# Optimization experiments

Measured on AMD Instinct MI355X. Metric: run time of the kernel, lower is better.

Reference implementation:

```python
import jax, jax.numpy as jnp
import numpy as np
import math

B, S, D, H = 2, 2048, 1024, 16
DK = D // H


def setup_inputs() -> dict:
    key = jax.random.key(0)
    ks = jax.random.split(key, 12)
    std = 1.0 / math.sqrt(D)
    inp = {
        "query": jax.random.normal(ks[0], (B, S, D), jnp.float32),
        "key_": jax.random.normal(ks[1], (B, S, D), jnp.float32),
        "value": jax.random.normal(ks[2], (B, S, D), jnp.float32),
        # causal mask: True = masked out
        "attn_mask": jnp.triu(jnp.ones((S, S), jnp.bool_), k=1),
        "w_q": jax.random.uniform(ks[3], (D, D), jnp.float32, -std, std),
        "b_q": jax.random.uniform(ks[4], (D,), jnp.float32, -std, std),
        "w_k": jax.random.uniform(ks[5], (D, D), jnp.float32, -std, std),
        "b_k": jax.random.uniform(ks[6], (D,), jnp.float32, -std, std),
        "w_v": jax.random.uniform(ks[7], (D, D), jnp.float32, -std, std),
        "b_v": jax.random.uniform(ks[8], (D,), jnp.float32, -std, std),
        "w_o": jax.random.uniform(ks[9], (D, D), jnp.float32, -std, std),
        "b_o": jax.random.uniform(ks[10], (D,), jnp.float32, -std, std),
    }
    return inp


def reference(query, key_, value, attn_mask, w_q, b_q, w_k, b_k, w_v, b_v, w_o, b_o):
    # linear projections (torch Linear: x @ W.T + b)
    q = query @ w_q.T + b_q
    k = key_ @ w_k.T + b_k
    v = value @ w_v.T + b_v
    # [B, H, S, DK]
    q = q.reshape(B, S, H, DK).transpose(0, 2, 1, 3)
    k = k.reshape(B, S, H, DK).transpose(0, 2, 1, 3)
    v = v.reshape(B, S, H, DK).transpose(0, 2, 1, 3)
    scores = jnp.einsum("bhqd,bhkd->bhqk", q, k) / jnp.sqrt(jnp.float32(DK))
    scores = jnp.where(attn_mask[None, None, :, :], -jnp.inf, scores)
    attn = jax.nn.softmax(scores, axis=-1)
    context = jnp.einsum("bhqk,bhkd->bhqd", attn, v)
    context = context.transpose(0, 2, 1, 3).reshape(B, S, D)
    return context @ w_o.T + b_o
```

## Files before the change

### kernel.cpp

```cpp
#include <hip/hip_runtime.h>

#define B_ 2
#define S_ 2048
#define D_ 1024
#define H_ 16
#define DK_ 64
#define K_ 1024

typedef __bf16 bf16x8 __attribute__((ext_vector_type(8)));
typedef __bf16 bf16x4 __attribute__((ext_vector_type(4)));
typedef float f32x4 __attribute__((ext_vector_type(4)));

#define QSCALE 0.18033688011112042f

__device__ __forceinline__ void gload16(const void* g, void* l) {
    __builtin_amdgcn_global_load_lds(
        (const __attribute__((address_space(1))) unsigned int*)g,
        (__attribute__((address_space(3))) unsigned int*)l, 16, 0, 0);
}

__device__ __forceinline__ bf16x8 cvt8f(const float* __restrict__ p) {
    f32x4 a = *reinterpret_cast<const f32x4*>(p);
    f32x4 b = *reinterpret_cast<const f32x4*>(p + 4);
    bf16x8 r;
#pragma unroll
    for (int j = 0; j < 4; ++j) { r[j] = (__bf16)a[j]; r[j + 4] = (__bf16)b[j]; }
    return r;
}

__global__ __launch_bounds__(256) void cvt_all(
    const float* __restrict__ s0, const float* __restrict__ s1, const float* __restrict__ s2,
    const float* __restrict__ s3, const float* __restrict__ s4, const float* __restrict__ s5,
    const float* __restrict__ s6,
    __bf16* __restrict__ d0, __bf16* __restrict__ d1, __bf16* __restrict__ d2,
    __bf16* __restrict__ d3, __bf16* __restrict__ d4, __bf16* __restrict__ d5,
    __bf16* __restrict__ d6)
{
    const int y = blockIdx.y;
    const float* s; __bf16* d; int n8;
    const int n8_big = (B_ * S_ * D_) / 8, n8_w = (D_ * D_) / 8;
    switch (y) {
        case 0: s = s0; d = d0; n8 = n8_big; break;
        case 1: s = s1; d = d1; n8 = n8_big; break;
        case 2: s = s2; d = d2; n8 = n8_big; break;
        case 3: s = s3; d = d3; n8 = n8_w; break;
        case 4: s = s4; d = d4; n8 = n8_w; break;
        case 5: s = s5; d = d5; n8 = n8_w; break;
        default: s = s6; d = d6; n8 = n8_w; break;
    }
    int i = blockIdx.x * 256 + threadIdx.x;
    if (i >= n8) return;
    *reinterpret_cast<bf16x8*>(d + (size_t)i * 8) = cvt8f(s + (size_t)i * 8);
}

__global__ __launch_bounds__(256) void gemm_qkv(
    const __bf16* __restrict__ qin, const __bf16* __restrict__ kin, const __bf16* __restrict__ vin,
    const __bf16* __restrict__ wq,  const __bf16* __restrict__ wk,  const __bf16* __restrict__ wv,
    const float* __restrict__ bq,   const float* __restrict__ bk,   const float* __restrict__ bv,
    __bf16* __restrict__ qo, __bf16* __restrict__ ko, __bf16* __restrict__ vto)
{
    __shared__ __attribute__((aligned(16))) __bf16 ldsA[2 * 128 * 32];
    __shared__ __attribute__((aligned(16))) __bf16 ldsB[2 * 128 * 32];

    const int z = blockIdx.z;
    const __bf16* A; const __bf16* Bm;
    int brow, bcol;
    if (z == 0)      { A = qin; Bm = wq;  brow = blockIdx.x * 128; bcol = blockIdx.y * 128; }
    else if (z == 1) { A = kin; Bm = wk;  brow = blockIdx.x * 128; bcol = blockIdx.y * 128; }
    else             { A = wv;  Bm = vin;
                       brow = (blockIdx.x & 7) * 128;
                       bcol = (blockIdx.y * 4 + (blockIdx.x >> 3)) * 128; }

    const int tid = threadIdx.x;
    const int w = tid >> 6, lane = tid & 63;
    const int l15 = lane & 15, lh = lane >> 4;
    const int wr = w >> 1, wc = w & 1;
    const int srow  = lane >> 2;
    const int scolb = (((lane & 3) ^ ((lane >> 3) & 3))) * 16;
    const char* Ab = (const char*)A;
    const char* Bb = (const char*)Bm;

    auto stage = [&](int buf, int k0) {
#pragma unroll
        for (int c = 0; c < 2; ++c) {
            const int chunk = w * 2 + c;
            const int row   = chunk * 16 + srow;
            const int loff  = __builtin_amdgcn_readfirstlane(buf * 8192 + chunk * 1024);
            gload16(Ab + (size_t)(brow + row) * 2048 + k0 * 2 + scolb, (char*)ldsA + loff);
            gload16(Bb + (size_t)(bcol + row) * 2048 + k0 * 2 + scolb, (char*)ldsB + loff);
        }
    };

    const int rsw = ((l15 >> 1) & 3);

    f32x4 acc[4][4] = {};
    stage(0, 0);
    int buf = 0;
    for (int k0 = 0; k0 < K_; k0 += 32) {
        if (k0 + 32 < K_) {
            stage(buf ^ 1, k0 + 32);
            asm volatile("s_waitcnt vmcnt(4)" ::: "memory");
        } else {
            asm volatile("s_waitcnt vmcnt(0)" ::: "memory");
        }
        __builtin_amdgcn_s_barrier();
        __builtin_amdgcn_sched_barrier(0);

        const int bo = buf * 8192;
        bf16x8 af[4], bfr[4];
#pragma unroll
        for (int m = 0; m < 4; ++m) {
            const int row = wr * 64 + m * 16 + l15;
            af[m] = *reinterpret_cast<const bf16x8*>(
                (const char*)ldsA + bo + row * 64 + ((lh ^ rsw) * 16));
        }
#pragma unroll
        for (int n = 0; n < 4; ++n) {
            const int row = wc * 64 + n * 16 + l15;
            bfr[n] = *reinterpret_cast<const bf16x8*>(
                (const char*)ldsB + bo + row * 64 + ((lh ^ rsw) * 16));
        }

        __builtin_amdgcn_s_setprio(1);
#pragma unroll
        for (int m = 0; m < 4; ++m)
#pragma unroll
            for (int n = 0; n < 4; ++n)
                acc[m][n] = __builtin_amdgcn_mfma_f32_16x16x32_bf16(bfr[n], af[m], acc[m][n], 0, 0, 0);
        __builtin_amdgcn_s_setprio(0);

        __builtin_amdgcn_s_barrier();
        buf ^= 1;
    }

    if (z < 2) {
        const float* bias = (z == 0) ? bq : bk;
        __bf16* o = (z == 0) ? qo : ko;
        const int hh  = (bcol >> 6) + wc;
#pragma unroll
        for (int ni = 0; ni < 4; ++ni) {
            const int n4  = bcol + wc * 64 + ni * 16 + lh * 4;
            const f32x4 b4 = *reinterpret_cast<const f32x4*>(bias + n4);
            const int dk4 = ni * 16 + lh * 4;
#pragma unroll
            for (int mi = 0; mi < 4; ++mi) {
                const int m  = brow + wr * 64 + mi * 16 + l15;
                const int bb = m >> 11, ss = m & (S_ - 1);
                bf16x4 pk;
#pragma unroll
                for (int r = 0; r < 4; ++r) {
                    float v = acc[mi][ni][r] + b4[r];
                    if (z == 0) v *= QSCALE;
                    pk[r] = (__bf16)v;
                }
                *reinterpret_cast<bf16x4*>(
                    o + (((size_t)(bb * H_ + hh)) * S_ + ss) * DK_ + dk4) = pk;
            }
        }
    } else {
#pragma unroll
        for (int mi = 0; mi < 4; ++mi) {
            const int m  = brow + wr * 64 + mi * 16 + l15;
            const int hh = m >> 6, dk = m & 63;
            const float bias = bv[m];
#pragma unroll
            for (int ni = 0; ni < 4; ++ni) {
                const int n4 = bcol + wc * 64 + ni * 16 + lh * 4;
                const int bb = n4 >> 11, ss = n4 & (S_ - 1);
                bf16x4 pk;
#pragma unroll
                for (int r = 0; r < 4; ++r)
                    pk[r] = (__bf16)(acc[mi][ni][r] + bias);
                *reinterpret_cast<bf16x4*>(
                    vto + (((size_t)(bb * H_ + hh)) * DK_ + dk) * S_ + ss) = pk;
            }
        }
    }
}

__global__ __launch_bounds__(256) void gemm_out(
    const __bf16* __restrict__ A, const __bf16* __restrict__ Bm,
    const float* __restrict__ bias, float* __restrict__ out)
{
    __shared__ __attribute__((aligned(16))) __bf16 ldsA[2 * 128 * 32];
    __shared__ __attribute__((aligned(16))) __bf16 ldsB[2 * 128 * 32];

    const int tid = threadIdx.x;
    const int w = tid >> 6, lane = tid & 63;
    const int l15 = lane & 15, lh = lane >> 4;
    const int wr = w >> 1, wc = w & 1;
    const int brow = blockIdx.x * 128;
    const int bcol = blockIdx.y * 128;
    const int srow  = lane >> 2;
    const int scolb = (((lane & 3) ^ ((lane >> 3) & 3))) * 16;
    const char* Ab = (const char*)A;
    const char* Bb = (const char*)Bm;

    auto stage = [&](int buf, int k0) {
#pragma unroll
        for (int c = 0; c < 2; ++c) {
            const int chunk = w * 2 + c;
            const int row   = chunk * 16 + srow;
            const int loff  = __builtin_amdgcn_readfirstlane(buf * 8192 + chunk * 1024);
            gload16(Ab + (size_t)(brow + row) * 2048 + k0 * 2 + scolb, (char*)ldsA + loff);
            gload16(Bb + (size_t)(bcol + row) * 2048 + k0 * 2 + scolb, (char*)ldsB + loff);
        }
    };

    const int rsw = ((l15 >> 1) & 3);

    f32x4 acc[4][4] = {};
    stage(0, 0);
    int buf = 0;
    for (int k0 = 0; k0 < K_; k0 += 32) {
        if (k0 + 32 < K_) {
            stage(buf ^ 1, k0 + 32);
            asm volatile("s_waitcnt vmcnt(4)" ::: "memory");
        } else {
            asm volatile("s_waitcnt vmcnt(0)" ::: "memory");
        }
        __builtin_amdgcn_s_barrier();
        __builtin_amdgcn_sched_barrier(0);

        const int bo = buf * 8192;
        bf16x8 af[4], bfr[4];
#pragma unroll
        for (int m = 0; m < 4; ++m) {
            const int row = wr * 64 + m * 16 + l15;
            af[m] = *reinterpret_cast<const bf16x8*>(
                (const char*)ldsA + bo + row * 64 + ((lh ^ rsw) * 16));
        }
#pragma unroll
        for (int n = 0; n < 4; ++n) {
            const int row = wc * 64 + n * 16 + l15;
            bfr[n] = *reinterpret_cast<const bf16x8*>(
                (const char*)ldsB + bo + row * 64 + ((lh ^ rsw) * 16));
        }

        __builtin_amdgcn_s_setprio(1);
#pragma unroll
        for (int m = 0; m < 4; ++m)
#pragma unroll
            for (int n = 0; n < 4; ++n)
                acc[m][n] = __builtin_amdgcn_mfma_f32_16x16x32_bf16(bfr[n], af[m], acc[m][n], 0, 0, 0);
        __builtin_amdgcn_s_setprio(0);

        __builtin_amdgcn_s_barrier();
        buf ^= 1;
    }

#pragma unroll
    for (int ni = 0; ni < 4; ++ni) {
        const int n4 = bcol + wc * 64 + ni * 16 + lh * 4;
        const f32x4 b4 = *reinterpret_cast<const f32x4*>(bias + n4);
#pragma unroll
        for (int mi = 0; mi < 4; ++mi) {
            const int m = brow + wr * 64 + mi * 16 + l15;
            f32x4 v;
#pragma unroll
            for (int r = 0; r < 4; ++r) v[r] = acc[mi][ni][r] + b4[r];
            *reinterpret_cast<f32x4*>(out + (size_t)m * D_ + n4) = v;
        }
    }
}

__global__ __launch_bounds__(256, 4) void attn_kernel(
    const __bf16* __restrict__ Q, const __bf16* __restrict__ K,
    const __bf16* __restrict__ VT, __bf16* __restrict__ CTX)
{
    __shared__ __attribute__((aligned(16))) char ldsK[2][8192];
    __shared__ __attribute__((aligned(16))) char ldsV[2][8192];
    __shared__ __attribute__((aligned(16))) __bf16 p_lds[4][16][64];

    const int tid = threadIdx.x;
    const int w = tid >> 6, l = tid & 63;
    const int l15 = l & 15, lh = l >> 4;

    const int c  = blockIdx.x & 255;
    const int rr = blockIdx.x >> 8;
    const int qq = c >> 5;
    const int bhidx = c & 31;
    int panel;
    if (rr == 0)      panel = 31 - qq;
    else if (rr == 1) panel = qq;
    else if (rr == 2) panel = 23 - qq;
    else              panel = 8 + qq;
    const int h = bhidx & 15;
    const int b = bhidx >> 4;

    const size_t bh = (size_t)(b * H_ + h);
    const __bf16* qp   = Q + bh * S_ * DK_;
    const char*  kbase = (const char*)(K  + bh * S_ * DK_);
    const char*  vbase = (const char*)(VT + bh * DK_ * S_);

    const int np = panel + 1;
    const int wave_base = panel * 64 + w * 16;

    const int srow = l >> 3;
    const int ssw  = ((l & 7) * 16) ^ (srow * 16);

    auto stage = [&](int pos) {
        const int k0 = pos * 64;
        char* lk = ldsK[pos & 1];
        char* lv = ldsV[pos & 1];
#pragma unroll
        for (int i = 0; i < 2; ++i) {
            const int r0   = w * 16 + i * 8;
            const int loff = __builtin_amdgcn_readfirstlane(r0 * 128);
            gload16(kbase + (size_t)(k0 + r0 + srow) * 128 + ssw, lk + loff);
            gload16(vbase + (size_t)(r0 + srow) * 4096 + (size_t)k0 * 2 + ssw, lv + loff);
        }
    };

    bf16x8 aq[2];
#pragma unroll
    for (int cc = 0; cc < 2; ++cc)
        aq[cc] = *reinterpret_cast<const bf16x8*>(
            qp + (size_t)(wave_base + l15) * DK_ + cc * 32 + lh * 8);

    bf16x8 vones;
#pragma unroll
    for (int j = 0; j < 8; ++j) vones[j] = (__bf16)1.0f;
    const f32x4 fzero = {0.f, 0.f, 0.f, 0.f};

    f32x4 acc[4] = {};
    f32x4 acc_l = {};
    float mrun = -INFINITY;

    stage(0);

    for (int it = 0; it < np; ++it) {
        if (it + 1 < np) {
            stage(it + 1);
            asm volatile("s_waitcnt vmcnt(4)" ::: "memory");
        } else {
            asm volatile("s_waitcnt vmcnt(0)" ::: "memory");
        }
        __builtin_amdgcn_s_barrier();
        __builtin_amdgcn_sched_barrier(0);

        const int k0 = it * 64;
        const char* lk = ldsK[it & 1];
        const char* lv = ldsV[it & 1];

        bf16x8 ak[4][2];
#pragma unroll
        for (int t = 0; t < 4; ++t)
#pragma unroll
            for (int cc = 0; cc < 2; ++cc) {
                const int col = (cc * 64 + lh * 16) ^ ((l15 & 7) << 4);
                ak[t][cc] = *reinterpret_cast<const bf16x8*>(lk + (t * 16 + l15) * 128 + col);
            }

        f32x4 sacc[4];
        __builtin_amdgcn_s_setprio(1);
#pragma unroll
        for (int t = 0; t < 4; ++t) {
            sacc[t] = __builtin_amdgcn_mfma_f32_16x16x32_bf16(ak[t][0], aq[0], fzero, 0, 0, 0);
            sacc[t] = __builtin_amdgcn_mfma_f32_16x16x32_bf16(ak[t][1], aq[1], sacc[t], 0, 0, 0);
        }
        __builtin_amdgcn_s_setprio(0);

        bf16x8 bv[4][2];
#pragma unroll
        for (int nt = 0; nt < 4; ++nt)
#pragma unroll
            for (int c2 = 0; c2 < 2; ++c2) {
                const int col = (c2 * 64 + lh * 16) ^ ((l15 & 7) << 4);
                bv[nt][c2] = *reinterpret_cast<const bf16x8*>(lv + (nt * 16 + l15) * 128 + col);
            }

        if (k0 + 63 > wave_base) {
            const int qa = wave_base + l15;
#pragma unroll
            for (int t = 0; t < 4; ++t)
#pragma unroll
                for (int r = 0; r < 4; ++r) {
                    const int ka = k0 + t * 16 + lh * 4 + r;
                    if (ka > qa) sacc[t][r] = -INFINITY;
                }
        }

        f32x4 m4 = sacc[0];
#pragma unroll
        for (int t = 1; t < 4; ++t)
#pragma unroll
            for (int r = 0; r < 4; ++r) m4[r] = fmaxf(m4[r], sacc[t][r]);
        float rm = fmaxf(fmaxf(m4[0], m4[1]), fmaxf(m4[2], m4[3]));
        rm = fmaxf(rm, __shfl_xor(rm, 16, 64));
        rm = fmaxf(rm, __shfl_xor(rm, 32, 64));

        if (!__all(rm <= mrun + 8.f)) {
            const float mnew = fmaxf(mrun, rm);
            const float scl  = exp2f(mrun - mnew);
            mrun = mnew;
#pragma unroll
            for (int r = 0; r < 4; ++r) {
                const float sr = __shfl(scl, lh * 4 + r, 64);
#pragma unroll
                for (int nt = 0; nt < 4; ++nt) acc[nt][r] *= sr;
                acc_l[r] *= sr;
            }
        }

#pragma unroll
        for (int t = 0; t < 4; ++t) {
            bf16x4 pk;
#pragma unroll
            for (int r = 0; r < 4; ++r)
                pk[r] = (__bf16)exp2f(sacc[t][r] - mrun);
            const int wcol = (t * 16 + lh * 4) ^ ((l15 & 7) << 3);
            *reinterpret_cast<bf16x4*>(&p_lds[w][l15][wcol]) = pk;
        }

        bf16x8 pa[2];
#pragma unroll
        for (int c2 = 0; c2 < 2; ++c2) {
            const int rcol = (c2 * 32 + lh * 8) ^ ((l15 & 7) << 3);
            pa[c2] = *reinterpret_cast<const bf16x8*>(&p_lds[w][l15][rcol]);
        }

        __builtin_amdgcn_s_setprio(1);
#pragma unroll
        for (int nt = 0; nt < 4; ++nt)
#pragma unroll
            for (int c2 = 0; c2 < 2; ++c2)
                acc[nt] = __builtin_amdgcn_mfma_f32_16x16x32_bf16(
                    pa[c2], bv[nt][c2], acc[nt], 0, 0, 0);
        acc_l = __builtin_amdgcn_mfma_f32_16x16x32_bf16(pa[0], vones, acc_l, 0, 0, 0);
        acc_l = __builtin_amdgcn_mfma_f32_16x16x32_bf16(pa[1], vones, acc_l, 0, 0, 0);
        __builtin_amdgcn_s_setprio(0);

        __builtin_amdgcn_s_barrier();
    }

#pragma unroll
    for (int r = 0; r < 4; ++r) {
        const float linv = 1.f / acc_l[r];
        const int srow2 = wave_base + lh * 4 + r;
#pragma unroll
        for (int nt = 0; nt < 4; ++nt)
            CTX[((size_t)b * S_ + srow2) * D_ + h * DK_ + nt * 16 + l15] =
                (__bf16)(acc[nt][r] * linv);
    }
}

extern "C" void kernel_launch(void* const* d_in, const int* in_sizes, int n_in,
                              void* d_out, int out_size, void* d_ws, size_t ws_size,
                              hipStream_t stream) {
    (void)in_sizes; (void)n_in; (void)out_size; (void)ws_size;

    const float* query = (const float*)d_in[0];
    const float* key_  = (const float*)d_in[1];
    const float* value = (const float*)d_in[2];
    const float* w_q = (const float*)d_in[4];
    const float* b_q = (const float*)d_in[5];
    const float* w_k = (const float*)d_in[6];
    const float* b_k = (const float*)d_in[7];
    const float* w_v = (const float*)d_in[8];
    const float* b_v = (const float*)d_in[9];
    const float* w_o = (const float*)d_in[10];
    const float* b_o = (const float*)d_in[11];
    float* out = (float*)d_out;

    char* Wp = (char*)d_ws;
    const size_t MB = 1024 * 1024;
    __bf16* qin = (__bf16*)(Wp + 0 * MB);
    __bf16* kin = (__bf16*)(Wp + 8 * MB);
    __bf16* vin = (__bf16*)(Wp + 16 * MB);
    __bf16* wq  = (__bf16*)(Wp + 24 * MB);
    __bf16* wk  = (__bf16*)(Wp + 26 * MB);
    __bf16* wv  = (__bf16*)(Wp + 28 * MB);
    __bf16* wo  = (__bf16*)(Wp + 30 * MB);
    __bf16* q   = (__bf16*)(Wp + 32 * MB);
    __bf16* k   = (__bf16*)(Wp + 40 * MB);
    __bf16* vt  = (__bf16*)(Wp + 48 * MB);
    __bf16* ctx = qin;

    const int n8_big = (B_ * S_ * D_) / 8;

    hipLaunchKernelGGL(cvt_all, dim3(n8_big / (256 * 8) * 8, 7), dim3(256), 0, stream,
                       query, key_, value, w_q, w_k, w_v, w_o,
                       qin, kin, vin, wq, wk, wv, wo);
    hipLaunchKernelGGL(gemm_qkv, dim3(32, 8, 3), dim3(256), 0, stream,
                       qin, kin, vin, wq, wk, wv, b_q, b_k, b_v, q, k, vt);
    hipLaunchKernelGGL(attn_kernel, dim3(1024), dim3(256), 0, stream,
                       q, k, vt, ctx);
    hipLaunchKernelGGL(gemm_out, dim3(32, 8), dim3(256), 0, stream,
                       ctx, wo, b_o, out);
}
```

Baseline: 131.0 us.

## Triple-buffer GEMM LDS pipeline and remap workgroups across XCDs

Both projection GEMMs now use three LDS buffers with a prefetch distance of two K-tiles. This drops the trailing barrier in each iteration, so only one barrier per K-step remains. The grids are flattened to 1D, and block IDs are remapped so that consecutive tiles land on the same XCD (wg&7 chiplet interleave), which is meant to improve L2 reuse of shared A/B panels. The cost is 48KB of LDS per block instead of 32KB, which may reduce occupancy.

Measured after the change: 133.5 us. No clear change (+1.9%).

```diff
diff --git a/kernel.cpp b/kernel.cpp
--- a/kernel.cpp
+++ b/kernel.cpp
@@ -59,17 +59,23 @@
     const float* __restrict__ bq,   const float* __restrict__ bk,   const float* __restrict__ bv,
     __bf16* __restrict__ qo, __bf16* __restrict__ ko, __bf16* __restrict__ vto)
 {
-    __shared__ __attribute__((aligned(16))) __bf16 ldsA[2 * 128 * 32];
-    __shared__ __attribute__((aligned(16))) __bf16 ldsB[2 * 128 * 32];
-
-    const int z = blockIdx.z;
+    __shared__ __attribute__((aligned(16))) char ldsA[3 * 8192];
+    __shared__ __attribute__((aligned(16))) char ldsB[3 * 8192];
+
+    const int wg   = blockIdx.x;
+    const int wgid = (wg & 7) * 96 + (wg >> 3);
+    const int z    = wgid >> 8;
+    const int rem  = wgid & 255;
+    const int by   = rem >> 5;
+    const int bx   = rem & 31;
+
     const __bf16* A; const __bf16* Bm;
     int brow, bcol;
-    if (z == 0)      { A = qin; Bm = wq;  brow = blockIdx.x * 128; bcol = blockIdx.y * 128; }
-    else if (z == 1) { A = kin; Bm = wk;  brow = blockIdx.x * 128; bcol = blockIdx.y * 128; }
+    if (z == 0)      { A = qin; Bm = wq;  brow = bx * 128; bcol = by * 128; }
+    else if (z == 1) { A = kin; Bm = wk;  brow = bx * 128; bcol = by * 128; }
     else             { A = wv;  Bm = vin;
-                       brow = (blockIdx.x & 7) * 128;
-                       bcol = (blockIdx.y * 4 + (blockIdx.x >> 3)) * 128; }
+                       brow = (bx & 7) * 128;
+                       bcol = (by * 4 + (bx >> 3)) * 128; }
 
     const int tid = threadIdx.x;
     const int w = tid >> 6, lane = tid & 63;
@@ -80,45 +86,46 @@
     const char* Ab = (const char*)A;
     const char* Bb = (const char*)Bm;
 
-    auto stage = [&](int buf, int k0) {
+    auto stage = [&](int tt, int buf) {
+        const int k0 = tt * 32;
 #pragma unroll
         for (int c = 0; c < 2; ++c) {
             const int chunk = w * 2 + c;
             const int row   = chunk * 16 + srow;
             const int loff  = __builtin_amdgcn_readfirstlane(buf * 8192 + chunk * 1024);
-            gload16(Ab + (size_t)(brow + row) * 2048 + k0 * 2 + scolb, (char*)ldsA + loff);
-            gload16(Bb + (size_t)(bcol + row) * 2048 + k0 * 2 + scolb, (char*)ldsB + loff);
+            gload16(Ab + (size_t)(brow + row) * 2048 + k0 * 2 + scolb, ldsA + loff);
+            gload16(Bb + (size_t)(bcol + row) * 2048 + k0 * 2 + scolb, ldsB + loff);
         }
     };
 
     const int rsw = ((l15 >> 1) & 3);
-
     f32x4 acc[4][4] = {};
-    stage(0, 0);
-    int buf = 0;
-    for (int k0 = 0; k0 < K_; k0 += 32) {
-        if (k0 + 32 < K_) {
-            stage(buf ^ 1, k0 + 32);
-            asm volatile("s_waitcnt vmcnt(4)" ::: "memory");
-        } else {
-            asm volatile("s_waitcnt vmcnt(0)" ::: "memory");
-        }
+    const int NT = K_ / 32;
+
+    stage(0, 0); stage(1, 1);
+    int cur = 0;
+    for (int t = 0; t < NT; ++t) {
+        if (t + 1 < NT) { asm volatile("s_waitcnt vmcnt(4)" ::: "memory"); }
+        else            { asm volatile("s_waitcnt vmcnt(0)" ::: "memory"); }
         __builtin_amdgcn_s_barrier();
         __builtin_amdgcn_sched_barrier(0);
 
-        const int bo = buf * 8192;
+        if (t + 2 < NT) {
+            const int sbuf = (cur == 0) ? 2 : cur - 1;
+            stage(t + 2, sbuf);
+        }
+
+        const int bo = cur * 8192;
         bf16x8 af[4], bfr[4];
 #pragma unroll
         for (int m = 0; m < 4; ++m) {
             const int row = wr * 64 + m * 16 + l15;
-            af[m] = *reinterpret_cast<const bf16x8*>(
-                (const char*)ldsA + bo + row * 64 + ((lh ^ rsw) * 16));
+            af[m] = *reinterpret_cast<const bf16x8*>(ldsA + bo + row * 64 + ((lh ^ rsw) * 16));
         }
 #pragma unroll
         for (int n = 0; n < 4; ++n) {
             const int row = wc * 64 + n * 16 + l15;
-            bfr[n] = *reinterpret_cast<const bf16x8*>(
-                (const char*)ldsB + bo + row * 64 + ((lh ^ rsw) * 16));
+            bfr[n] = *reinterpret_cast<const bf16x8*>(ldsB + bo + row * 64 + ((lh ^ rsw) * 16));
         }
 
         __builtin_amdgcn_s_setprio(1);
@@ -129,14 +136,13 @@
                 acc[m][n] = __builtin_amdgcn_mfma_f32_16x16x32_bf16(bfr[n], af[m], acc[m][n], 0, 0, 0);
         __builtin_amdgcn_s_setprio(0);
 
-        __builtin_amdgcn_s_barrier();
-        buf ^= 1;
+        cur = (cur == 2) ? 0 : cur + 1;
     }
 
     if (z < 2) {
         const float* bias = (z == 0) ? bq : bk;
         __bf16* o = (z == 0) ? qo : ko;
-        const int hh  = (bcol >> 6) + wc;
+        const int hh = (bcol >> 6) + wc;
 #pragma unroll
         for (int ni = 0; ni < 4; ++ni) {
             const int n4  = bcol + wc * 64 + ni * 16 + lh * 4;
@@ -182,59 +188,65 @@
     const __bf16* __restrict__ A, const __bf16* __restrict__ Bm,
     const float* __restrict__ bias, float* __restrict__ out)
 {
-    __shared__ __attribute__((aligned(16))) __bf16 ldsA[2 * 128 * 32];
-    __shared__ __attribute__((aligned(16))) __bf16 ldsB[2 * 128 * 32];
+    __shared__ __attribute__((aligned(16))) char ldsA[3 * 8192];
+    __shared__ __attribute__((aligned(16))) char ldsB[3 * 8192];
+
+    const int wg   = blockIdx.x;
+    const int wgid = (wg & 7) * 32 + (wg >> 3);
+    const int by   = wgid >> 5;
+    const int bx   = wgid & 31;
+    const int brow = bx * 128;
+    const int bcol = by * 128;
 
     const int tid = threadIdx.x;
     const int w = tid >> 6, lane = tid & 63;
     const int l15 = lane & 15, lh = lane >> 4;
     const int wr = w >> 1, wc = w & 1;
-    const int brow = blockIdx.x * 128;
-    const int bcol = blockIdx.y * 128;
     const int srow  = lane >> 2;
     const int scolb = (((lane & 3) ^ ((lane >> 3) & 3))) * 16;
     const char* Ab = (const char*)A;
     const char* Bb = (const char*)Bm;
 
-    auto stage = [&](int buf, int k0) {
+    auto stage = [&](int tt, int buf) {
+        const int k0 = tt * 32;
 #pragma unroll
         for (int c = 0; c < 2; ++c) {
             const int chunk = w * 2 + c;
             const int row   = chunk * 16 + srow;
             const int loff  = __builtin_amdgcn_readfirstlane(buf * 8192 + chunk * 1024);
-            gload16(Ab + (size_t)(brow + row) * 2048 + k0 * 2 + scolb, (char*)ldsA + loff);
-            gload16(Bb + (size_t)(bcol + row) * 2048 + k0 * 2 + scolb, (char*)ldsB + loff);
+            gload16(Ab + (size_t)(brow + row) * 2048 + k0 * 2 + scolb, ldsA + loff);
+            gload16(Bb + (size_t)(bcol + row) * 2048 + k0 * 2 + scolb, ldsB + loff);
         }
     };
 
     const int rsw = ((l15 >> 1) & 3);
-
     f32x4 acc[4][4] = {};
-    stage(0, 0);
-    int buf = 0;
-    for (int k0 = 0; k0 < K_; k0 += 32) {
-        if (k0 + 32 < K_) {
-            stage(buf ^ 1, k0 + 32);
-            asm volatile("s_waitcnt vmcnt(4)" ::: "memory");
-        } else {
-            asm volatile("s_waitcnt vmcnt(0)" ::: "memory");
-        }
+    const int NT = K_ / 32;
+
+    stage(0, 0); stage(1, 1);
+    int cur = 0;
+    for (int t = 0; t < NT; ++t) {
+        if (t + 1 < NT) { asm volatile("s_waitcnt vmcnt(4)" ::: "memory"); }
+        else            { asm volatile("s_waitcnt vmcnt(0)" ::: "memory"); }
         __builtin_amdgcn_s_barrier();
         __builtin_amdgcn_sched_barrier(0);
 
-        const int bo = buf * 8192;
+        if (t + 2 < NT) {
+            const int sbuf = (cur == 0) ? 2 : cur - 1;
+            stage(t + 2, sbuf);
+        }
+
+        const int bo = cur * 8192;
         bf16x8 af[4], bfr[4];
 #pragma unroll
         for (int m = 0; m < 4; ++m) {
             const int row = wr * 64 + m * 16 + l15;
-            af[m] = *reinterpret_cast<const bf16x8*>(
-                (const char*)ldsA + bo + row * 64 + ((lh ^ rsw) * 16));
+            af[m] = *reinterpret_cast<const bf16x8*>(ldsA + bo + row * 64 + ((lh ^ rsw) * 16));
         }
 #pragma unroll
         for (int n = 0; n < 4; ++n) {
             const int row = wc * 64 + n * 16 + l15;
-            bfr[n] = *reinterpret_cast<const bf16x8*>(
-                (const char*)ldsB + bo + row * 64 + ((lh ^ rsw) * 16));
+            bfr[n] = *reinterpret_cast<const bf16x8*>(ldsB + bo + row * 64 + ((lh ^ rsw) * 16));
         }
 
         __builtin_amdgcn_s_setprio(1);
@@ -245,8 +257,7 @@
                 acc[m][n] = __builtin_amdgcn_mfma_f32_16x16x32_bf16(bfr[n], af[m], acc[m][n], 0, 0, 0);
         __builtin_amdgcn_s_setprio(0);
 
-        __builtin_amdgcn_s_barrier();
-        buf ^= 1;
+        cur = (cur == 2) ? 0 : cur + 1;
     }
 
 #pragma unroll
@@ -482,10 +493,10 @@
     hipLaunchKernelGGL(cvt_all, dim3(n8_big / (256 * 8) * 8, 7), dim3(256), 0, stream,
                        query, key_, value, w_q, w_k, w_v, w_o,
                        qin, kin, vin, wq, wk, wv, wo);
-    hipLaunchKernelGGL(gemm_qkv, dim3(32, 8, 3), dim3(256), 0, stream,
+    hipLaunchKernelGGL(gemm_qkv, dim3(768), dim3(256), 0, stream,
                        qin, kin, vin, wq, wk, wv, b_q, b_k, b_v, q, k, vt);
     hipLaunchKernelGGL(attn_kernel, dim3(1024), dim3(256), 0, stream,
                        q, k, vt, ctx);
-    hipLaunchKernelGGL(gemm_out, dim3(32, 8), dim3(256), 0, stream,
+    hipLaunchKernelGGL(gemm_out, dim3(256), dim3(256), 0, stream,
                        ctx, wo, b_o, out);
 }
```

## Rewrite QKV GEMM with 256x256 tiles, 8-wave blocks and deep LDS pipeline

Applied to the files above, without the earlier changes.

Replaces the 128x128, 4-wave QKV projection GEMM with a 256x256-tile, 8-wave kernel. It uses a 128KB LDS ring of eight 16KB slots, a multi-stage prefetch scheme with phased barriers and vmcnt waits, and a remapped 1D grid of 192 blocks that groups tiles per XCD. The output GEMM also gets a 1D grid with XCD-aware block remapping. The aim is more data reuse per loaded tile and better latency hiding. The cost is fewer blocks (192 on a 256-CU part), higher register and LDS pressure, and complex synchronisation.

New measurement: 119.9 us, median of 2. 8.5% less time.

```diff
diff --git a/kernel.cpp b/kernel.cpp
--- a/kernel.cpp
+++ b/kernel.cpp
@@ -53,98 +53,134 @@
     *reinterpret_cast<bf16x8*>(d + (size_t)i * 8) = cvt8f(s + (size_t)i * 8);
 }
 
-__global__ __launch_bounds__(256) void gemm_qkv(
+__global__ __launch_bounds__(512, 2) void gemm_qkv8(
     const __bf16* __restrict__ qin, const __bf16* __restrict__ kin, const __bf16* __restrict__ vin,
     const __bf16* __restrict__ wq,  const __bf16* __restrict__ wk,  const __bf16* __restrict__ wv,
     const float* __restrict__ bq,   const float* __restrict__ bk,   const float* __restrict__ bv,
     __bf16* __restrict__ qo, __bf16* __restrict__ ko, __bf16* __restrict__ vto)
 {
-    __shared__ __attribute__((aligned(16))) __bf16 ldsA[2 * 128 * 32];
-    __shared__ __attribute__((aligned(16))) __bf16 ldsB[2 * 128 * 32];
-
-    const int z = blockIdx.z;
-    const __bf16* A; const __bf16* Bm;
-    int brow, bcol;
-    if (z == 0)      { A = qin; Bm = wq;  brow = blockIdx.x * 128; bcol = blockIdx.y * 128; }
-    else if (z == 1) { A = kin; Bm = wk;  brow = blockIdx.x * 128; bcol = blockIdx.y * 128; }
-    else             { A = wv;  Bm = vin;
-                       brow = (blockIdx.x & 7) * 128;
-                       bcol = (blockIdx.y * 4 + (blockIdx.x >> 3)) * 128; }
+    __shared__ __attribute__((aligned(128))) char lds[8 * 16384];
 
     const int tid = threadIdx.x;
     const int w = tid >> 6, lane = tid & 63;
     const int l15 = lane & 15, lh = lane >> 4;
-    const int wr = w >> 1, wc = w & 1;
-    const int srow  = lane >> 2;
-    const int scolb = (((lane & 3) ^ ((lane >> 3) & 3))) * 16;
+    const int wr = w >> 2, wc = w & 3;
+
+    const int wg   = blockIdx.x;
+    const int wgid = (wg & 7) * 24 + (wg >> 3);
+    const int z    = wgid >> 6;
+    const int rem  = wgid & 63;
+
+    const __bf16* A; const __bf16* Bm;
+    if (z == 0)      { A = qin; Bm = wq; }
+    else if (z == 1) { A = kin; Bm = wk; }
+    else             { A = wv;  Bm = vin; }
+    int brow, bcol;
+    if (z < 2) { brow = (rem & 15) * 256; bcol = (rem >> 4) * 256; }
+    else       { brow = (rem & 3)  * 256; bcol = (rem >> 2) * 256; }
+
     const char* Ab = (const char*)A;
     const char* Bb = (const char*)Bm;
-
-    auto stage = [&](int buf, int k0) {
-#pragma unroll
-        for (int c = 0; c < 2; ++c) {
-            const int chunk = w * 2 + c;
-            const int row   = chunk * 16 + srow;
-            const int loff  = __builtin_amdgcn_readfirstlane(buf * 8192 + chunk * 1024);
-            gload16(Ab + (size_t)(brow + row) * 2048 + k0 * 2 + scolb, (char*)ldsA + loff);
-            gload16(Bb + (size_t)(bcol + row) * 2048 + k0 * 2 + scolb, (char*)ldsB + loff);
+    const int abase = brow * 2048;
+    const int bbase = bcol * 2048;
+
+    int soff[2];
+#pragma unroll
+    for (int j = 0; j < 2; ++j) {
+        const int s = j * 512 + tid;
+        const int row = s >> 2, cslot = s & 3;
+        const int cswz = cslot ^ (((row >> 3) & 1) << 1);
+        soff[j] = row * 2048 + cswz * 16;
+    }
+
+    auto stageHT = [&](int g, int slot) {
+        const int u = g >> 2, kind = g & 3;
+        const char* src = (kind & 1) ? Bb : Ab;
+        const int base = ((kind & 1) ? bbase : abase) + u * 128 + (kind >> 1) * 64;
+#pragma unroll
+        for (int j = 0; j < 2; ++j) {
+            const int ldst = __builtin_amdgcn_readfirstlane(slot * 16384 + j * 8192 + w * 1024);
+            gload16(src + (size_t)(base + soff[j]), (char*)lds + ldst);
         }
     };
 
-    const int rsw = ((l15 >> 1) & 3);
-
-    f32x4 acc[4][4] = {};
-    stage(0, 0);
-    int buf = 0;
-    for (int k0 = 0; k0 < K_; k0 += 32) {
-        if (k0 + 32 < K_) {
-            stage(buf ^ 1, k0 + 32);
-            asm volatile("s_waitcnt vmcnt(4)" ::: "memory");
-        } else {
-            asm volatile("s_waitcnt vmcnt(0)" ::: "memory");
-        }
-        __builtin_amdgcn_s_barrier();
-        __builtin_amdgcn_sched_barrier(0);
-
-        const int bo = buf * 8192;
-        bf16x8 af[4], bfr[4];
-#pragma unroll
-        for (int m = 0; m < 4; ++m) {
-            const int row = wr * 64 + m * 16 + l15;
-            af[m] = *reinterpret_cast<const bf16x8*>(
-                (const char*)ldsA + bo + row * 64 + ((lh ^ rsw) * 16));
-        }
-#pragma unroll
-        for (int n = 0; n < 4; ++n) {
-            const int row = wc * 64 + n * 16 + l15;
-            bfr[n] = *reinterpret_cast<const bf16x8*>(
-                (const char*)ldsB + bo + row * 64 + ((lh ^ rsw) * 16));
-        }
-
-        __builtin_amdgcn_s_setprio(1);
-#pragma unroll
-        for (int m = 0; m < 4; ++m)
-#pragma unroll
-            for (int n = 0; n < 4; ++n)
-                acc[m][n] = __builtin_amdgcn_mfma_f32_16x16x32_bf16(bfr[n], af[m], acc[m][n], 0, 0, 0);
-        __builtin_amdgcn_s_setprio(0);
-
-        __builtin_amdgcn_s_barrier();
-        buf ^= 1;
-    }
+    const int ainner = (l15 * 64 + lh * 16) ^ ((l15 & 8) << 2);
+
+    f32x4 acc[8][4] = {};
+    bf16x8 bfr[4];
+
+    stageHT(0, 0); stageHT(1, 1); stageHT(2, 2);
+    stageHT(3, 3); stageHT(4, 4); stageHT(5, 5);
+    asm volatile("s_waitcnt vmcnt(8)" ::: "memory");
+    __builtin_amdgcn_s_barrier();
+
+#define PHASE(PAR, KS, MH, RDB, P)                                                   \
+    {                                                                                \
+        bf16x8 af[4];                                                                \
+        _Pragma("unroll")                                                            \
+        for (int q = 0; q < 4; ++q)                                                  \
+            af[q] = *reinterpret_cast<const bf16x8*>(                                \
+                lds + ((PAR) * 4 + (KS) * 2) * 16384 + (wr * 8 + (MH) * 4 + q) * 1024 + ainner); \
+        if (RDB) {                                                                   \
+            _Pragma("unroll")                                                        \
+            for (int q = 0; q < 4; ++q)                                              \
+                bfr[q] = *reinterpret_cast<const bf16x8*>(                           \
+                    lds + ((PAR) * 4 + (KS) * 2 + 1) * 16384 + (wc * 4 + q) * 1024 + ainner); \
+        }                                                                            \
+        { const int g = 8 * i + 6 + (P); if (g < 64) stageHT(g, (6 + (P)) & 7); }    \
+        __builtin_amdgcn_s_barrier();                                                \
+        asm volatile("s_waitcnt lgkmcnt(0)" ::: "memory");                           \
+        __builtin_amdgcn_sched_barrier(0);                                           \
+        __builtin_amdgcn_s_setprio(1);                                               \
+        _Pragma("unroll")                                                            \
+        for (int q = 0; q < 4; ++q)                                                  \
+            _Pragma("unroll")                                                        \
+            for (int n = 0; n < 4; ++n)                                              \
+                acc[(MH) * 4 + q][n] = __builtin_amdgcn_mfma_f32_16x16x32_bf16(      \
+                    bfr[n], af[q], acc[(MH) * 4 + q][n], 0, 0, 0);                   \
+        __builtin_amdgcn_s_setprio(0);                                               \
+    }
+
+    for (int i = 0; i < 8; ++i) {
+        const bool last = (i == 7);
+        PHASE(0, 0, 0, 1, 0);
+        __builtin_amdgcn_s_barrier();
+        PHASE(0, 0, 1, 0, 1);
+        asm volatile("s_waitcnt vmcnt(6)" ::: "memory");
+        __builtin_amdgcn_s_barrier();
+        PHASE(0, 1, 0, 1, 2);
+        __builtin_amdgcn_s_barrier();
+        PHASE(0, 1, 1, 0, 3);
+        if (!last) { asm volatile("s_waitcnt vmcnt(6)" ::: "memory"); }
+        else       { asm volatile("s_waitcnt vmcnt(4)" ::: "memory"); }
+        __builtin_amdgcn_s_barrier();
+        PHASE(1, 0, 0, 1, 4);
+        __builtin_amdgcn_s_barrier();
+        PHASE(1, 0, 1, 0, 5);
+        if (!last) { asm volatile("s_waitcnt vmcnt(6)" ::: "memory"); }
+        else       { asm volatile("s_waitcnt vmcnt(0)" ::: "memory"); }
+        __builtin_amdgcn_s_barrier();
+        PHASE(1, 1, 0, 1, 6);
+        __builtin_amdgcn_s_barrier();
+        PHASE(1, 1, 1, 0, 7);
+        if (!last) {
+            asm volatile("s_waitcnt vmcnt(6)" ::: "memory");
+            __builtin_amdgcn_s_barrier();
+        }
+    }
+#undef PHASE
 
     if (z < 2) {
         const float* bias = (z == 0) ? bq : bk;
         __bf16* o = (z == 0) ? qo : ko;
-        const int hh  = (bcol >> 6) + wc;
 #pragma unroll
         for (int ni = 0; ni < 4; ++ni) {
             const int n4  = bcol + wc * 64 + ni * 16 + lh * 4;
             const f32x4 b4 = *reinterpret_cast<const f32x4*>(bias + n4);
-            const int dk4 = ni * 16 + lh * 4;
-#pragma unroll
-            for (int mi = 0; mi < 4; ++mi) {
-                const int m  = brow + wr * 64 + mi * 16 + l15;
+            const int hh = n4 >> 6, dk4 = n4 & 63;
+#pragma unroll
+            for (int mi = 0; mi < 8; ++mi) {
+                const int m  = brow + wr * 128 + mi * 16 + l15;
                 const int bb = m >> 11, ss = m & (S_ - 1);
                 bf16x4 pk;
 #pragma unroll
@@ -159,8 +195,8 @@
         }
     } else {
 #pragma unroll
-        for (int mi = 0; mi < 4; ++mi) {
-            const int m  = brow + wr * 64 + mi * 16 + l15;
+        for (int mi = 0; mi < 8; ++mi) {
+            const int m  = brow + wr * 128 + mi * 16 + l15;
             const int hh = m >> 6, dk = m & 63;
             const float bias = bv[m];
 #pragma unroll
@@ -185,12 +221,17 @@
     __shared__ __attribute__((aligned(16))) __bf16 ldsA[2 * 128 * 32];
     __shared__ __attribute__((aligned(16))) __bf16 ldsB[2 * 128 * 32];
 
+    const int wg   = blockIdx.x;
+    const int wgid = (wg & 7) * 32 + (wg >> 3);
+    const int by   = wgid >> 5;
+    const int bx   = wgid & 31;
+    const int brow = bx * 128;
+    const int bcol = by * 128;
+
     const int tid = threadIdx.x;
     const int w = tid >> 6, lane = tid & 63;
     const int l15 = lane & 15, lh = lane >> 4;
     const int wr = w >> 1, wc = w & 1;
-    const int brow = blockIdx.x * 128;
-    const int bcol = blockIdx.y * 128;
     const int srow  = lane >> 2;
     const int scolb = (((lane & 3) ^ ((lane >> 3) & 3))) * 16;
     const char* Ab = (const char*)A;
@@ -482,10 +523,10 @@
     hipLaunchKernelGGL(cvt_all, dim3(n8_big / (256 * 8) * 8, 7), dim3(256), 0, stream,
                        query, key_, value, w_q, w_k, w_v, w_o,
                        qin, kin, vin, wq, wk, wv, wo);
-    hipLaunchKernelGGL(gemm_qkv, dim3(32, 8, 3), dim3(256), 0, stream,
+    hipLaunchKernelGGL(gemm_qkv8, dim3(192), dim3(512), 0, stream,
                        qin, kin, vin, wq, wk, wv, b_q, b_k, b_v, q, k, vt);
     hipLaunchKernelGGL(attn_kernel, dim3(1024), dim3(256), 0, stream,
                        q, k, vt, ctx);
-    hipLaunchKernelGGL(gemm_out, dim3(32, 8), dim3(256), 0, stream,
+    hipLaunchKernelGGL(gemm_out, dim3(256), dim3(256), 0, stream,
                        ctx, wo, b_o, out);
 }
```
